# Performance work log

Hardware: AMD Instinct MI355X
Metric: run time of the kernel (lower is better)

The kernel has to match this reference:

```python
import jax, jax.numpy as jnp
import numpy as np
from jax import lax

_DN = ('NCHW', 'OIHW', 'NCHW')

def _lenet(x, w1, b1, w2, b2):
    # Conv2d(k=5) -> ReLU -> MaxPool(2,2) -> Conv2d(k=5) -> ReLU -> MaxPool(2,2) -> Flatten
    y = lax.conv_general_dilated(x, w1, (1, 1), 'VALID', dimension_numbers=_DN) + b1[None, :, None, None]
    y = jax.nn.relu(y)
    y = lax.reduce_window(y, -jnp.inf, lax.max, (1, 1, 2, 2), (1, 1, 2, 2), 'VALID')
    y = lax.conv_general_dilated(y, w2, (1, 1), 'VALID', dimension_numbers=_DN) + b2[None, :, None, None]
    y = jax.nn.relu(y)
    y = lax.reduce_window(y, -jnp.inf, lax.max, (1, 1, 2, 2), (1, 1, 2, 2), 'VALID')
    return y.reshape(y.shape[0], -1)  # (N, 16*5*5=400)


def setup_inputs() -> dict:
    key = jax.random.key(0)
    ks = jax.random.split(key, 16)
    n, S = 1024, 8
    n_data, n_classes, hid = 50000, 10, 12
    in_feats = 400
    sc = lambda fan_in: 1.0 / np.sqrt(fan_in)
    return {
        'img': jax.random.normal(ks[0], (n, 3, 32, 32), jnp.float32),
        'train': jax.random.normal(ks[1], (n_data, 3, 32, 32), jnp.float32),
        'mem': jax.random.normal(ks[2], (n_data, n_classes), jnp.float32),
        'w1': jax.random.normal(ks[3], (6, 3, 5, 5), jnp.float32) * sc(3 * 25),
        'b1': jax.random.normal(ks[4], (6,), jnp.float32) * sc(3 * 25),
        'w2': jax.random.normal(ks[5], (16, 6, 5, 5), jnp.float32) * sc(6 * 25),
        'b2': jax.random.normal(ks[6], (16,), jnp.float32) * sc(6 * 25),
        'Wf': jax.random.normal(ks[7], (hid, in_feats), jnp.float32) * sc(in_feats),
        'bf': jax.random.normal(ks[8], (hid,), jnp.float32) * sc(in_feats),
        'Wg': jax.random.normal(ks[9], (hid * n_classes, in_feats), jnp.float32) * sc(in_feats),
        'bg': jax.random.normal(ks[10], (hid * n_classes,), jnp.float32) * sc(in_feats),
        'Wm': jax.random.normal(ks[11], (n_classes, n_classes), jnp.float32) * sc(n_classes),
        'bm': jax.random.normal(ks[12], (n_classes,), jnp.float32) * sc(n_classes),
        'idx': jax.random.randint(ks[13], (n,), 0, n_data, jnp.int64) if jax.config.jax_enable_x64 else jax.random.randint(ks[13], (n,), 0, n_data).astype(jnp.int32),
        'refs': jax.random.randint(ks[14], (n, S), 0, n_data).astype(jnp.int32),
    }


def reference(img, train, mem, w1, b1, w2, b2, Wf, bf, Wg, bg, Wm, bm, idx, refs):
    n, S = refs.shape
    H = bf.shape[0]          # hid_feats
    C = bm.shape[0]          # n_classes
    feat = _lenet(img, w1, b1, w2, b2)                       # (n, 400)
    x = feat @ Wf.T + bf                                     # pos(img): (n, H)
    ref_feat = _lenet(train[refs.reshape(-1)], w1, b1, w2, b2)
    ref_x = (ref_feat @ Wf.T + bf).reshape(n, S, H)          # pos(train[refs])
    diff = x[:, None, :] - ref_x                             # (n, S, H)
    grad = (feat @ Wg.T + bg).reshape(n, H, C)               # field(img)
    logits = mem[refs] @ Wm.T + bm + jnp.einsum('nsh,nhc->nsc', diff, grad)  # (n, S, C)
    dist = jax.nn.softmax(-jnp.linalg.norm(diff, axis=-1), axis=-1)          # (n, S)
    logits = jnp.concatenate([logits, jnp.zeros((n, 1, C), logits.dtype)], axis=1)
    dist = jnp.concatenate([dist, jnp.zeros((n, 1), dist.dtype)], axis=1)
    return jnp.einsum('nsc,ns->nc', logits, dist)            # (n, C)
```

## Files before the change

kernel.cpp:

```cpp
#include <hip/hip_runtime.h>
#include <math.h>

__device__ float g_feat[9216 * 400];

__global__ __launch_bounds__(256, 2) void lenet_kernel(
    const float* __restrict__ img,
    const float* __restrict__ train,
    const int* __restrict__ refs,
    const float* __restrict__ w1, const float* __restrict__ b1,
    const float* __restrict__ w2, const float* __restrict__ b2)
{
    __shared__ __align__(16) float s_in[3 * 32 * 32];
    __shared__ __align__(16) float s_p1[6 * 14 * 32];

    const int blk = blockIdx.x;
    const int tid = threadIdx.x;

    const float* src = (blk < 1024)
        ? (img + (size_t)blk * 3072)
        : (train + (size_t)refs[blk - 1024] * 3072);
    const float4* src4 = (const float4*)src;

    #pragma unroll
    for (int j = 0; j < 3; ++j) {
        const int i4 = tid + j * 256;
        const float4 v = src4[i4];
        const int ic   = i4 >> 8;
        const int row  = (i4 >> 3) & 31;
        const int slot = i4 & 7;
        *(float4*)(s_in + ic * 1024 + row * 32 + ((slot ^ (row & 7)) << 2)) = v;
    }
    __syncthreads();

    if (tid < 98) {
        const int py = tid / 7;
        const int xt = tid - py * 7;
        const int r0 = py * 2;

        #pragma unroll 1
        for (int och = 0; och < 2; ++och) {
            float acc[3][2][4];
            #pragma unroll
            for (int o = 0; o < 3; ++o) {
                const float b = b1[och * 3 + o];
                #pragma unroll
                for (int r = 0; r < 2; ++r)
                    #pragma unroll
                    for (int j = 0; j < 4; ++j) acc[o][r][j] = b;
            }

            #pragma unroll 1
            for (int ic = 0; ic < 3; ++ic) {
                const float* base = s_in + ic * 1024;
                const float* wic  = w1 + och * 3 * 75 + ic * 25;
                float A[8], B[8];
                {
                    const int row = r0, r7 = row & 7;
                    const float4 lo = *(const float4*)(base + row * 32 + ((xt ^ r7) << 2));
                    const float4 hi = *(const float4*)(base + row * 32 + (((xt + 1) ^ r7) << 2));
                    A[0]=lo.x; A[1]=lo.y; A[2]=lo.z; A[3]=lo.w;
                    A[4]=hi.x; A[5]=hi.y; A[6]=hi.z; A[7]=hi.w;
                }
                #pragma unroll
                for (int ky = 0; ky < 5; ++ky) {
                    const int row = r0 + ky + 1, r7 = row & 7;
                    const float4 lo = *(const float4*)(base + row * 32 + ((xt ^ r7) << 2));
                    const float4 hi = *(const float4*)(base + row * 32 + (((xt + 1) ^ r7) << 2));
                    B[0]=lo.x; B[1]=lo.y; B[2]=lo.z; B[3]=lo.w;
                    B[4]=hi.x; B[5]=hi.y; B[6]=hi.z; B[7]=hi.w;
                    #pragma unroll
                    for (int o = 0; o < 3; ++o) {
                        #pragma unroll
                        for (int kx = 0; kx < 5; ++kx) {
                            const float w = wic[o * 75 + ky * 5 + kx];
                            #pragma unroll
                            for (int j = 0; j < 4; ++j) {
                                acc[o][0][j] = fmaf(A[j + kx], w, acc[o][0][j]);
                                acc[o][1][j] = fmaf(B[j + kx], w, acc[o][1][j]);
                            }
                        }
                    }
                    #pragma unroll
                    for (int q = 0; q < 8; ++q) A[q] = B[q];
                }
            }

            const int r7 = py & 7;
            const int px0 = xt * 2;
            #pragma unroll
            for (int o = 0; o < 3; ++o) {
                const int oc = och * 3 + o;
                const float m0 = fmaxf(fmaxf(acc[o][0][0], acc[o][0][1]),
                                       fmaxf(acc[o][1][0], acc[o][1][1]));
                const float m1 = fmaxf(fmaxf(acc[o][0][2], acc[o][0][3]),
                                       fmaxf(acc[o][1][2], acc[o][1][3]));
                float* d = s_p1 + oc * 448 + py * 32 + (((px0 >> 2) ^ r7) << 2) + (px0 & 3);
                *(float2*)d = make_float2(fmaxf(m0, 0.0f), fmaxf(m1, 0.0f));
            }
        }
    }
    __syncthreads();

    if (tid < 160) {
        const int oc = tid / 10;
        const int oy = tid - oc * 10;

        float acc[10];
        {
            const float b = b2[oc];
            #pragma unroll
            for (int j = 0; j < 10; ++j) acc[j] = b;
        }
        const float* wrow = w2 + oc * 150;
        #pragma unroll 1
        for (int ic = 0; ic < 6; ++ic) {
            const float* base = s_p1 + ic * 448;
            const float* wic  = wrow + ic * 25;
            #pragma unroll
            for (int ky = 0; ky < 5; ++ky) {
                const int row = oy + ky, r7 = row & 7;
                const float* rb = base + row * 32;
                float in[14];
                const float4 q0 = *(const float4*)(rb + ((0 ^ r7) << 2));
                const float4 q1 = *(const float4*)(rb + ((1 ^ r7) << 2));
                const float4 q2 = *(const float4*)(rb + ((2 ^ r7) << 2));
                const float2 q3 = *(const float2*)(rb + ((3 ^ r7) << 2));
                in[0]=q0.x;  in[1]=q0.y;  in[2]=q0.z;  in[3]=q0.w;
                in[4]=q1.x;  in[5]=q1.y;  in[6]=q1.z;  in[7]=q1.w;
                in[8]=q2.x;  in[9]=q2.y;  in[10]=q2.z; in[11]=q2.w;
                in[12]=q3.x; in[13]=q3.y;
                #pragma unroll
                for (int kx = 0; kx < 5; ++kx) {
                    const float w = wic[ky * 5 + kx];
                    #pragma unroll
                    for (int j = 0; j < 10; ++j)
                        acc[j] = fmaf(in[j + kx], w, acc[j]);
                }
            }
        }
        float v[5];
        #pragma unroll
        for (int k = 0; k < 5; ++k) v[k] = fmaxf(acc[2 * k], acc[2 * k + 1]);
        float* fo = g_feat + (size_t)blk * 400 + oc * 25 + (oy >> 1) * 5;
        #pragma unroll
        for (int k = 0; k < 5; ++k) {
            const float m = fmaxf(v[k], __shfl_down(v[k], 1));
            if ((oy & 1) == 0) fo[k] = fmaxf(m, 0.0f);
        }
    }
}

__global__ __launch_bounds__(256) void head_kernel(
    const float* __restrict__ mem,
    const float* __restrict__ Wf, const float* __restrict__ bf,
    const float* __restrict__ Wg, const float* __restrict__ bg,
    const float* __restrict__ Wm, const float* __restrict__ bm,
    const int* __restrict__ refs,
    float* __restrict__ out)
{
    const int n = blockIdx.x;
    const int tid = threadIdx.x;

    __shared__ __align__(16) float s_feat[400];
    __shared__ __align__(16) float s_rfeat[8 * 400];
    __shared__ float s_x[12];
    __shared__ float s_rx[96];
    __shared__ float s_grad[120];
    __shared__ float s_diff[96];
    __shared__ float s_dist[8];
    __shared__ float s_logits[80];

    const float4* f4 = (const float4*)(g_feat + (size_t)n * 400);
    for (int i = tid; i < 100; i += 256) ((float4*)s_feat)[i] = f4[i];
    const float4* r4 = (const float4*)(g_feat + (size_t)(1024 + n * 8) * 400);
    for (int i = tid; i < 800; i += 256) ((float4*)s_rfeat)[i] = r4[i];
    __syncthreads();

    const int grp = tid >> 4;
    const int l16 = tid & 15;
    for (int r = 0; r < 15; ++r) {
        const int o = r * 16 + grp;
        if (o < 228) {
            const float* w;
            const float* f;
            if (o < 12)       { w = Wf + o * 400;              f = s_feat; }
            else if (o < 108) { const int t = o - 12;
                                w = Wf + (t % 12) * 400;       f = s_rfeat + (t / 12) * 400; }
            else              { const int g = o - 108;
                                w = Wg + g * 400;              f = s_feat; }
            float a = 0.0f;
            #pragma unroll
            for (int it = 0; it < 7; ++it) {
                const int k = it * 64 + l16 * 4;
                if (k < 400) {
                    const float4 wv = *(const float4*)(w + k);
                    const float4 fv = *(const float4*)(f + k);
                    a = fmaf(wv.x, fv.x, a); a = fmaf(wv.y, fv.y, a);
                    a = fmaf(wv.z, fv.z, a); a = fmaf(wv.w, fv.w, a);
                }
            }
            #pragma unroll
            for (int m = 8; m; m >>= 1) a += __shfl_xor(a, m);
            if (l16 == 0) {
                if (o < 12)       s_x[o] = a + bf[o];
                else if (o < 108) { const int t = o - 12; s_rx[t] = a + bf[t % 12]; }
                else              { const int g = o - 108; s_grad[g] = a + bg[g]; }
            }
        }
    }
    __syncthreads();

    if (tid < 96) {
        const int h = tid % 12;
        s_diff[tid] = s_x[h] - s_rx[tid];
    }
    __syncthreads();

    if (tid < 8) {
        float nn = 0.0f;
        #pragma unroll
        for (int h = 0; h < 12; ++h) { const float d = s_diff[tid * 12 + h]; nn += d * d; }
        s_dist[tid] = -sqrtf(nn);
    }
    if (tid == 0) {
        float mx = s_dist[0];
        #pragma unroll
        for (int s = 1; s < 8; ++s) mx = fmaxf(mx, s_dist[s]);
        float e[8]; float tot = 0.0f;
        #pragma unroll
        for (int s = 0; s < 8; ++s) { e[s] = expf(s_dist[s] - mx); tot += e[s]; }
        #pragma unroll
        for (int s = 0; s < 8; ++s) s_dist[s] = e[s] / tot;
    }
    if (tid < 80) {
        const int s = tid / 10, c = tid - s * 10;
        const float* mrow = mem + (size_t)refs[n * 8 + s] * 10;
        float a = bm[c];
        #pragma unroll
        for (int k = 0; k < 10; ++k) a += mrow[k] * Wm[c * 10 + k];
        #pragma unroll
        for (int h = 0; h < 12; ++h) a += s_diff[s * 12 + h] * s_grad[h * 10 + c];
        s_logits[tid] = a;
    }
    __syncthreads();

    if (tid < 10) {
        float a = 0.0f;
        #pragma unroll
        for (int s = 0; s < 8; ++s) a += s_dist[s] * s_logits[s * 10 + tid];
        out[n * 10 + tid] = a;
    }
}

extern "C" void kernel_launch(void* const* d_in, const int* in_sizes, int n_in,
                              void* d_out, int out_size, void* d_ws, size_t ws_size,
                              hipStream_t stream) {
    const float* img   = (const float*)d_in[0];
    const float* train = (const float*)d_in[1];
    const float* mem   = (const float*)d_in[2];
    const float* w1    = (const float*)d_in[3];
    const float* b1    = (const float*)d_in[4];
    const float* w2    = (const float*)d_in[5];
    const float* b2    = (const float*)d_in[6];
    const float* Wf    = (const float*)d_in[7];
    const float* bf    = (const float*)d_in[8];
    const float* Wg    = (const float*)d_in[9];
    const float* bg    = (const float*)d_in[10];
    const float* Wm    = (const float*)d_in[11];
    const float* bm    = (const float*)d_in[12];
    const int*   refs  = (const int*)d_in[14];
    float* out = (float*)d_out;

    lenet_kernel<<<9216, 256, 0, stream>>>(img, train, refs, w1, b1, w2, b2);
    head_kernel<<<1024, 256, 0, stream>>>(mem, Wf, bf, Wg, bg, Wm, bm, refs, out);
}
```

Before: 854.5 us.

## Spread LeNet conv work across all four waves and batch head over four samples

Conv1 work is redistributed so each of the four wavefronts handles half the pooled positions for one group of three output channels, instead of 98 threads in two waves looping over both channel groups. Conv2 threads are likewise spread so every wave gets 40 active lanes instead of leaving two waves idle. The head kernel now processes four samples per 512-thread block, so each Wf/Wg row is reused across more feature vectors and fewer blocks are launched. The cost is more shared memory in the head kernel and an index remap whose pairing of shuffled lanes must stay correct.

```diff
diff --git a/kernel.cpp b/kernel.cpp
--- a/kernel.cpp
+++ b/kernel.cpp
@@ -15,6 +15,8 @@
 
     const int blk = blockIdx.x;
     const int tid = threadIdx.x;
+    const int lane = tid & 63;
+    const int wv   = tid >> 6;
 
     const float* src = (blk < 1024)
         ? (img + (size_t)blk * 3072)
@@ -32,78 +34,79 @@
     }
     __syncthreads();
 
-    if (tid < 98) {
-        const int py = tid / 7;
-        const int xt = tid - py * 7;
-        const int r0 = py * 2;
+    if (lane < 49) {
+        const int och = wv >> 1;
+        const int pos = lane * 2 + (wv & 1);
+        const int py  = pos / 7;
+        const int xt  = pos - py * 7;
+        const int r0  = py * 2;
+
+        float acc[3][2][4];
+        #pragma unroll
+        for (int o = 0; o < 3; ++o) {
+            const float b = b1[och * 3 + o];
+            #pragma unroll
+            for (int r = 0; r < 2; ++r)
+                #pragma unroll
+                for (int j = 0; j < 4; ++j) acc[o][r][j] = b;
+        }
 
         #pragma unroll 1
-        for (int och = 0; och < 2; ++och) {
-            float acc[3][2][4];
-            #pragma unroll
-            for (int o = 0; o < 3; ++o) {
-                const float b = b1[och * 3 + o];
+        for (int ic = 0; ic < 3; ++ic) {
+            const float* base = s_in + ic * 1024;
+            const float* wic  = w1 + och * 3 * 75 + ic * 25;
+            float A[8], B[8];
+            {
+                const int row = r0, r7 = row & 7;
+                const float4 lo = *(const float4*)(base + row * 32 + ((xt ^ r7) << 2));
+                const float4 hi = *(const float4*)(base + row * 32 + (((xt + 1) ^ r7) << 2));
+                A[0]=lo.x; A[1]=lo.y; A[2]=lo.z; A[3]=lo.w;
+                A[4]=hi.x; A[5]=hi.y; A[6]=hi.z; A[7]=hi.w;
+            }
+            #pragma unroll
+            for (int ky = 0; ky < 5; ++ky) {
+                const int row = r0 + ky + 1, r7 = row & 7;
+                const float4 lo = *(const float4*)(base + row * 32 + ((xt ^ r7) << 2));
+                const float4 hi = *(const float4*)(base + row * 32 + (((xt + 1) ^ r7) << 2));
+                B[0]=lo.x; B[1]=lo.y; B[2]=lo.z; B[3]=lo.w;
+                B[4]=hi.x; B[5]=hi.y; B[6]=hi.z; B[7]=hi.w;
                 #pragma unroll
-                for (int r = 0; r < 2; ++r)
+                for (int o = 0; o < 3; ++o) {
                     #pragma unroll
-                    for (int j = 0; j < 4; ++j) acc[o][r][j] = b;
-            }
-
-            #pragma unroll 1
-            for (int ic = 0; ic < 3; ++ic) {
-                const float* base = s_in + ic * 1024;
-                const float* wic  = w1 + och * 3 * 75 + ic * 25;
-                float A[8], B[8];
-                {
-                    const int row = r0, r7 = row & 7;
-                    const float4 lo = *(const float4*)(base + row * 32 + ((xt ^ r7) << 2));
-                    const float4 hi = *(const float4*)(base + row * 32 + (((xt + 1) ^ r7) << 2));
-                    A[0]=lo.x; A[1]=lo.y; A[2]=lo.z; A[3]=lo.w;
-                    A[4]=hi.x; A[5]=hi.y; A[6]=hi.z; A[7]=hi.w;
+                    for (int kx = 0; kx < 5; ++kx) {
+                        const float w = wic[o * 75 + ky * 5 + kx];
+                        #pragma unroll
+                        for (int j = 0; j < 4; ++j) {
+                            acc[o][0][j] = fmaf(A[j + kx], w, acc[o][0][j]);
+                            acc[o][1][j] = fmaf(B[j + kx], w, acc[o][1][j]);
+                        }
+                    }
                 }
                 #pragma unroll
-                for (int ky = 0; ky < 5; ++ky) {
-                    const int row = r0 + ky + 1, r7 = row & 7;
-                    const float4 lo = *(const float4*)(base + row * 32 + ((xt ^ r7) << 2));
-                    const float4 hi = *(const float4*)(base + row * 32 + (((xt + 1) ^ r7) << 2));
-                    B[0]=lo.x; B[1]=lo.y; B[2]=lo.z; B[3]=lo.w;
-                    B[4]=hi.x; B[5]=hi.y; B[6]=hi.z; B[7]=hi.w;
-                    #pragma unroll
-                    for (int o = 0; o < 3; ++o) {
-                        #pragma unroll
-                        for (int kx = 0; kx < 5; ++kx) {
-                            const float w = wic[o * 75 + ky * 5 + kx];
-                            #pragma unroll
-                            for (int j = 0; j < 4; ++j) {
-                                acc[o][0][j] = fmaf(A[j + kx], w, acc[o][0][j]);
-                                acc[o][1][j] = fmaf(B[j + kx], w, acc[o][1][j]);
-                            }
-                        }
-                    }
-                    #pragma unroll
-                    for (int q = 0; q < 8; ++q) A[q] = B[q];
-                }
-            }
-
-            const int r7 = py & 7;
-            const int px0 = xt * 2;
-            #pragma unroll
-            for (int o = 0; o < 3; ++o) {
-                const int oc = och * 3 + o;
-                const float m0 = fmaxf(fmaxf(acc[o][0][0], acc[o][0][1]),
-                                       fmaxf(acc[o][1][0], acc[o][1][1]));
-                const float m1 = fmaxf(fmaxf(acc[o][0][2], acc[o][0][3]),
-                                       fmaxf(acc[o][1][2], acc[o][1][3]));
-                float* d = s_p1 + oc * 448 + py * 32 + (((px0 >> 2) ^ r7) << 2) + (px0 & 3);
-                *(float2*)d = make_float2(fmaxf(m0, 0.0f), fmaxf(m1, 0.0f));
-            }
-        }
-    }
-    __syncthreads();
-
-    if (tid < 160) {
-        const int oc = tid / 10;
-        const int oy = tid - oc * 10;
+                for (int q = 0; q < 8; ++q) A[q] = B[q];
+            }
+        }
+
+        const int r7 = py & 7;
+        const int px0 = xt * 2;
+        #pragma unroll
+        for (int o = 0; o < 3; ++o) {
+            const int oc = och * 3 + o;
+            const float m0 = fmaxf(fmaxf(acc[o][0][0], acc[o][0][1]),
+                                   fmaxf(acc[o][1][0], acc[o][1][1]));
+            const float m1 = fmaxf(fmaxf(acc[o][0][2], acc[o][0][3]),
+                                   fmaxf(acc[o][1][2], acc[o][1][3]));
+            float* d = s_p1 + oc * 448 + py * 32 + (((px0 >> 2) ^ r7) << 2) + (px0 & 3);
+            *(float2*)d = make_float2(fmaxf(m0, 0.0f), fmaxf(m1, 0.0f));
+        }
+    }
+    __syncthreads();
+
+    if (lane < 40) {
+        const int q  = (lane >> 1) * 4 + wv;
+        const int w  = q * 2 + (lane & 1);
+        const int oc = w / 10;
+        const int oy = w - oc * 10;
 
         float acc[10];
         {
@@ -131,10 +134,10 @@
                 in[12]=q3.x; in[13]=q3.y;
                 #pragma unroll
                 for (int kx = 0; kx < 5; ++kx) {
-                    const float w = wic[ky * 5 + kx];
+                    const float wgt = wic[ky * 5 + kx];
                     #pragma unroll
                     for (int j = 0; j < 10; ++j)
-                        acc[j] = fmaf(in[j + kx], w, acc[j]);
+                        acc[j] = fmaf(in[j + kx], wgt, acc[j]);
                 }
             }
         }
@@ -145,12 +148,12 @@
         #pragma unroll
         for (int k = 0; k < 5; ++k) {
             const float m = fmaxf(v[k], __shfl_down(v[k], 1));
-            if ((oy & 1) == 0) fo[k] = fmaxf(m, 0.0f);
+            if ((lane & 1) == 0) fo[k] = fmaxf(m, 0.0f);
         }
     }
 }
 
-__global__ __launch_bounds__(256) void head_kernel(
+__global__ __launch_bounds__(512) void head_kernel(
     const float* __restrict__ mem,
     const float* __restrict__ Wf, const float* __restrict__ bf,
     const float* __restrict__ Wg, const float* __restrict__ bg,
@@ -158,97 +161,118 @@
     const int* __restrict__ refs,
     float* __restrict__ out)
 {
-    const int n = blockIdx.x;
+    const int blk = blockIdx.x;
     const int tid = threadIdx.x;
-
-    __shared__ __align__(16) float s_feat[400];
-    __shared__ __align__(16) float s_rfeat[8 * 400];
-    __shared__ float s_x[12];
-    __shared__ float s_rx[96];
-    __shared__ float s_grad[120];
-    __shared__ float s_diff[96];
-    __shared__ float s_dist[8];
-    __shared__ float s_logits[80];
-
-    const float4* f4 = (const float4*)(g_feat + (size_t)n * 400);
-    for (int i = tid; i < 100; i += 256) ((float4*)s_feat)[i] = f4[i];
-    const float4* r4 = (const float4*)(g_feat + (size_t)(1024 + n * 8) * 400);
-    for (int i = tid; i < 800; i += 256) ((float4*)s_rfeat)[i] = r4[i];
+    const int n0  = blk * 4;
+
+    __shared__ __align__(16) float s_f[36 * 400];
+    __shared__ float s_out[4 * 228];
+    __shared__ float s_diff[4 * 96];
+    __shared__ float s_dist[4 * 8];
+    __shared__ float s_logits[4 * 80];
+
+    for (int i = tid; i < 3600; i += 512) {
+        const int r = i / 100, c = i - r * 100;
+        const int n_l = r / 9, v = r - n_l * 9;
+        const float* srcp = (v == 0)
+            ? (g_feat + (size_t)(n0 + n_l) * 400)
+            : (g_feat + (size_t)(1024 + (n0 + n_l) * 8 + (v - 1)) * 400);
+        *(float4*)(s_f + r * 400 + c * 4) = *(const float4*)(srcp + c * 4);
+    }
     __syncthreads();
 
     const int grp = tid >> 4;
     const int l16 = tid & 15;
-    for (int r = 0; r < 15; ++r) {
-        const int o = r * 16 + grp;
-        if (o < 228) {
+    for (int t = 0; t < 29; ++t) {
+        const int d = t * 32 + grp;
+        if (d < 912) {
             const float* w;
             const float* f;
-            if (o < 12)       { w = Wf + o * 400;              f = s_feat; }
-            else if (o < 108) { const int t = o - 12;
-                                w = Wf + (t % 12) * 400;       f = s_rfeat + (t / 12) * 400; }
-            else              { const int g = o - 108;
-                                w = Wg + g * 400;              f = s_feat; }
+            if (d < 432) {
+                const int h = d / 36, vec = d - h * 36;
+                w = Wf + h * 400;  f = s_f + vec * 400;
+            } else {
+                const int e = d - 432;
+                const int rg = e >> 2, n_l = e & 3;
+                w = Wg + rg * 400; f = s_f + n_l * 9 * 400;
+            }
             float a = 0.0f;
             #pragma unroll
             for (int it = 0; it < 7; ++it) {
                 const int k = it * 64 + l16 * 4;
                 if (k < 400) {
-                    const float4 wv = *(const float4*)(w + k);
-                    const float4 fv = *(const float4*)(f + k);
-                    a = fmaf(wv.x, fv.x, a); a = fmaf(wv.y, fv.y, a);
-                    a = fmaf(wv.z, fv.z, a); a = fmaf(wv.w, fv.w, a);
+                    const float4 wvv = *(const float4*)(w + k);
+                    const float4 fv  = *(const float4*)(f + k);
+                    a = fmaf(wvv.x, fv.x, a); a = fmaf(wvv.y, fv.y, a);
+                    a = fmaf(wvv.z, fv.z, a); a = fmaf(wvv.w, fv.w, a);
                 }
             }
             #pragma unroll
             for (int m = 8; m; m >>= 1) a += __shfl_xor(a, m);
             if (l16 == 0) {
-                if (o < 12)       s_x[o] = a + bf[o];
-                else if (o < 108) { const int t = o - 12; s_rx[t] = a + bf[t % 12]; }
-                else              { const int g = o - 108; s_grad[g] = a + bg[g]; }
-            }
-        }
-    }
-    __syncthreads();
-
-    if (tid < 96) {
-        const int h = tid % 12;
-        s_diff[tid] = s_x[h] - s_rx[tid];
-    }
-    __syncthreads();
-
-    if (tid < 8) {
+                if (d < 432) {
+                    const int h = d / 36, vec = d - h * 36;
+                    const int n_l = vec / 9, v = vec - n_l * 9;
+                    s_out[n_l * 228 + (v == 0 ? h : 12 + (v - 1) * 12 + h)] = a + bf[h];
+                } else {
+                    const int e = d - 432;
+                    const int rg = e >> 2, n_l = e & 3;
+                    s_out[n_l * 228 + 108 + rg] = a + bg[rg];
+                }
+            }
+        }
+    }
+    __syncthreads();
+
+    if (tid < 384) {
+        const int n_l = tid / 96, i = tid - n_l * 96;
+        const int h = i % 12;
+        s_diff[tid] = s_out[n_l * 228 + h] - s_out[n_l * 228 + 12 + i];
+    }
+    __syncthreads();
+
+    if (tid < 32) {
+        const int n_l = tid >> 3, s = tid & 7;
         float nn = 0.0f;
         #pragma unroll
-        for (int h = 0; h < 12; ++h) { const float d = s_diff[tid * 12 + h]; nn += d * d; }
+        for (int h = 0; h < 12; ++h) {
+            const float dd = s_diff[n_l * 96 + s * 12 + h];
+            nn = fmaf(dd, dd, nn);
+        }
         s_dist[tid] = -sqrtf(nn);
     }
-    if (tid == 0) {
-        float mx = s_dist[0];
-        #pragma unroll
-        for (int s = 1; s < 8; ++s) mx = fmaxf(mx, s_dist[s]);
+    if (tid < 4) {
+        float mx = s_dist[tid * 8];
+        #pragma unroll
+        for (int s = 1; s < 8; ++s) mx = fmaxf(mx, s_dist[tid * 8 + s]);
         float e[8]; float tot = 0.0f;
         #pragma unroll
-        for (int s = 0; s < 8; ++s) { e[s] = expf(s_dist[s] - mx); tot += e[s]; }
-        #pragma unroll
-        for (int s = 0; s < 8; ++s) s_dist[s] = e[s] / tot;
-    }
-    if (tid < 80) {
-        const int s = tid / 10, c = tid - s * 10;
-        const float* mrow = mem + (size_t)refs[n * 8 + s] * 10;
+        for (int s = 0; s < 8; ++s) { e[s] = expf(s_dist[tid * 8 + s] - mx); tot += e[s]; }
+        #pragma unroll
+        for (int s = 0; s < 8; ++s) s_dist[tid * 8 + s] = e[s] / tot;
+    }
+
+    if (tid < 320) {
+        const int n_l = tid / 80, r = tid - n_l * 80;
+        const int s = r / 10, c = r - s * 10;
+        const float* mrow = mem + (size_t)refs[(n0 + n_l) * 8 + s] * 10;
         float a = bm[c];
         #pragma unroll
-        for (int k = 0; k < 10; ++k) a += mrow[k] * Wm[c * 10 + k];
-        #pragma unroll
-        for (int h = 0; h < 12; ++h) a += s_diff[s * 12 + h] * s_grad[h * 10 + c];
-        s_logits[tid] = a;
-    }
-    __syncthreads();
-
-    if (tid < 10) {
+        for (int k = 0; k < 10; ++k) a = fmaf(mrow[k], Wm[c * 10 + k], a);
+        #pragma unroll
+        for (int h = 0; h < 12; ++h)
+            a = fmaf(s_diff[n_l * 96 + s * 12 + h], s_out[n_l * 228 + 108 + h * 10 + c], a);
+        s_logits[n_l * 80 + r] = a;
+    }
+    __syncthreads();
+
+    if (tid < 40) {
+        const int n_l = tid / 10, c = tid - n_l * 10;
         float a = 0.0f;
         #pragma unroll
-        for (int s = 0; s < 8; ++s) a += s_dist[s] * s_logits[s * 10 + tid];
-        out[n * 10 + tid] = a;
+        for (int s = 0; s < 8; ++s)
+            a = fmaf(s_dist[n_l * 8 + s], s_logits[n_l * 80 + s * 10 + c], a);
+        out[(n0 + n_l) * 10 + c] = a;
     }
 }
 
@@ -272,5 +296,5 @@
     float* out = (float*)d_out;
 
     lenet_kernel<<<9216, 256, 0, stream>>>(img, train, refs, w1, b1, w2, b2);
-    head_kernel<<<1024, 256, 0, stream>>>(mem, Wf, bf, Wg, bg, Wm, bm, refs, out);
+    head_kernel<<<256, 512, 0, stream>>>(mem, Wf, bf, Wg, bg, Wm, bm, refs, out);
 }
```

After: 886.3 us. 3.7% more time.
